# Kernel optimization log

Hardware: AMD Instinct MI355X
Metric: run time of the kernel (lower is better)

The kernel has to match this reference:

```python
import jax, jax.numpy as jnp
import numpy as np

B, L, D, E, H, TOP_K = 4, 2048, 1024, 8, 512, 2

def setup_inputs() -> dict:
    key = jax.random.key(0)
    k = jax.random.split(key, 6)
    x = jax.random.normal(k[0], (B, L, D), dtype=jnp.float32)
    gate_w = jax.random.normal(k[1], (D, E), dtype=jnp.float32) * 0.02
    gate_b = jnp.zeros((E,), jnp.float32)
    w1 = jax.random.normal(k[2], (E, D, H), dtype=jnp.float32) * 0.02
    b1 = jnp.zeros((E, H), jnp.float32)
    w2 = jax.random.normal(k[3], (E, H, D), dtype=jnp.float32) * 0.02
    b2 = jnp.zeros((E, D), jnp.float32)
    return {"x": x, "gate_w": gate_w, "gate_b": gate_b,
            "w1": w1, "b1": b1, "w2": w2, "b2": b2}

def reference(x, gate_w, gate_b, w1, b1, w2, b2):
    b, l, d = x.shape
    e = gate_w.shape[1]
    xf = x.reshape(-1, d)                      # [T, D], T = B*L
    t = xf.shape[0]
    # gating (eval mode: clean logits, no noise)
    logits = xf @ gate_w + gate_b              # [T, E]
    top_vals, top_idx = jax.lax.top_k(logits, TOP_K)
    top_gates = jax.nn.softmax(top_vals, axis=-1)
    gates = jnp.zeros((t, e), x.dtype).at[jnp.arange(t)[:, None], top_idx].set(top_gates)
    # per-expert 2-layer MLP computed densely, combined with sparse gates
    h = jax.nn.gelu(jnp.einsum('td,edh->eth', xf, w1) + b1[:, None, :], approximate=False)
    eo = jnp.einsum('eth,ehd->etd', h, w2) + b2[:, None, :]   # [E, T, D]
    out = jnp.einsum('te,etd->td', gates, eo)                 # weighted combine
    return out.reshape(b, l, d)
```

## Files before the change

kernel.cpp:

```cpp
#include <hip/hip_runtime.h>
#include <hip/hip_bf16.h>
#include <stdint.h>

#define B_    4
#define L_    2048
#define T_    8192
#define D_    1024
#define E_    8
#define H_    512

typedef __bf16  bf16x8 __attribute__((ext_vector_type(8)));
typedef float   f32x4  __attribute__((ext_vector_type(4)));
typedef unsigned short ushort_t;

__device__ __forceinline__ ushort_t f2bf(float f) {
    union { float f; unsigned u; } v; v.f = f;
    unsigned u = v.u;
    unsigned r = (u + 0x7fffu + ((u >> 16) & 1u)) >> 16;
    return (ushort_t)r;
}

__device__ __forceinline__ float gelu_exact(float v) {
    return 0.5f * v * (1.0f + erff(v * 0.70710678118654752f));
}

__device__ __forceinline__ void gld_lds16(const void* g, void* l) {
    __attribute__((address_space(3))) uint32_t* lp =
        reinterpret_cast<__attribute__((address_space(3))) uint32_t*>(
            reinterpret_cast<uintptr_t>(l));
    const __attribute__((address_space(1))) uint32_t* gp =
        reinterpret_cast<const __attribute__((address_space(1))) uint32_t*>(
            reinterpret_cast<uintptr_t>(g));
    __builtin_amdgcn_global_load_lds(gp, lp, 16, 0, 0);
}

__global__ __launch_bounds__(256) void transpose_cvt2(
    const float* __restrict__ w1, const float* __restrict__ w2,
    ushort_t* __restrict__ o1, ushort_t* __restrict__ o2)
{
    __shared__ float tile[32][33];
    const int mz = blockIdx.y;
    const float* src; ushort_t* dst; int C, R, sh;
    if (mz < E_) {
        src = w1 + (size_t)mz * D_ * H_; dst = o1 + (size_t)mz * D_ * H_;
        R = D_; C = H_; sh = 4;
    } else {
        const int m = mz - E_;
        src = w2 + (size_t)m * D_ * H_;  dst = o2 + (size_t)m * D_ * H_;
        R = H_; C = D_; sh = 5;
    }
    const int bx = blockIdx.x & ((1 << sh) - 1);
    const int by = blockIdx.x >> sh;
    const int r0 = by * 32, c0 = bx * 32;
    const int tid = threadIdx.x;
    const int lr = tid >> 3;
    const int lc = (tid & 7) * 4;
    float4 v = *(const float4*)(src + (size_t)(r0 + lr) * C + c0 + lc);
    tile[lr][lc+0] = v.x; tile[lr][lc+1] = v.y;
    tile[lr][lc+2] = v.z; tile[lr][lc+3] = v.w;
    __syncthreads();
    ushort4 o;
    o.x = f2bf(tile[lc+0][lr]);
    o.y = f2bf(tile[lc+1][lr]);
    o.z = f2bf(tile[lc+2][lr]);
    o.w = f2bf(tile[lc+3][lr]);
    *(ushort4*)(dst + (size_t)(c0 + lr) * R + r0 + lc) = o;
}

__global__ __launch_bounds__(256) void gating_kernel(
    const float* __restrict__ x, const float* __restrict__ gw,
    const float* __restrict__ gb,
    int* __restrict__ eidx, float* __restrict__ gsel, ushort_t* __restrict__ xbf)
{
    __shared__ float gwT[E_][D_];
    const int tid = threadIdx.x;

    #pragma unroll
    for (int it = 0; it < 8; ++it) {
        const int idx = it * 256 + tid;
        float4 v = *(const float4*)(gw + (size_t)idx * 4);
        const int row = idx >> 1;
        const int col = (idx & 1) * 4;
        gwT[col+0][row] = v.x;
        gwT[col+1][row] = v.y;
        gwT[col+2][row] = v.z;
        gwT[col+3][row] = v.w;
    }
    __syncthreads();

    const int wave = tid >> 6;
    const int lane = tid & 63;

    #pragma unroll
    for (int it = 0; it < 2; ++it) {
        const int t = blockIdx.x * 8 + wave * 2 + it;
        const float* xr = x + (size_t)t * D_;
        ushort_t* xbr = xbf + (size_t)t * D_;

        float acc[E_];
        #pragma unroll
        for (int e = 0; e < E_; ++e) acc[e] = 0.f;

        #pragma unroll
        for (int j = 0; j < 4; ++j) {
            const int d = j * 256 + lane * 4;
            float4 xv = *(const float4*)(xr + d);
            ushort4 o;
            o.x = f2bf(xv.x); o.y = f2bf(xv.y); o.z = f2bf(xv.z); o.w = f2bf(xv.w);
            *(ushort4*)(xbr + d) = o;
            #pragma unroll
            for (int e = 0; e < E_; ++e) {
                float4 w = *(const float4*)(&gwT[e][d]);
                acc[e] += xv.x * w.x + xv.y * w.y + xv.z * w.z + xv.w * w.w;
            }
        }
        #pragma unroll
        for (int s = 1; s < 64; s <<= 1) {
            #pragma unroll
            for (int e = 0; e < E_; ++e)
                acc[e] += __shfl_xor(acc[e], s, 64);
        }
        if (lane == 0) {
            float v[E_];
            #pragma unroll
            for (int e = 0; e < E_; ++e) v[e] = acc[e] + gb[e];
            int i0 = 0;
            #pragma unroll
            for (int e = 1; e < E_; ++e) if (v[e] > v[i0]) i0 = e;
            int i1 = (i0 == 0) ? 1 : 0;
            #pragma unroll
            for (int e = 0; e < E_; ++e) if (e != i0 && v[e] > v[i1]) i1 = e;
            float g0 = 1.f / (1.f + expf(v[i1] - v[i0]));
            eidx[t] = i0 | (i1 << 8);
            gsel[t] = g0;
        }
    }
}

__global__ __launch_bounds__(256) void bucket_kernel(
    const int* __restrict__ eidx, const float* __restrict__ gsel,
    int* __restrict__ counts, int* __restrict__ btok, float* __restrict__ bgate,
    uint32_t* __restrict__ tpos)
{
    __shared__ int lcnt[E_];
    __shared__ int lbase[E_];
    const int tid = threadIdx.x;
    if (tid < E_) lcnt[tid] = 0;
    __syncthreads();
    const int t = blockIdx.x * 256 + tid;
    const int pk = eidx[t];
    const float g0 = gsel[t];
    const int i0 = pk & 0xff, i1 = (pk >> 8) & 0xff;
    const int p0 = atomicAdd(&lcnt[i0], 1);
    const int p1 = atomicAdd(&lcnt[i1], 1);
    __syncthreads();
    if (tid < E_) lbase[tid] = atomicAdd(&counts[tid], lcnt[tid]);
    __syncthreads();
    const int q0 = lbase[i0] + p0, q1 = lbase[i1] + p1;
    btok[i0 * T_ + q0] = t; bgate[i0 * T_ + q0] = g0;
    btok[i1 * T_ + q1] = t; bgate[i1 * T_ + q1] = 1.f - g0;
    tpos[t] = (uint32_t)((i0 << 13) | q0) | ((uint32_t)((i1 << 13) | q1) << 16);
}

__global__ __launch_bounds__(256) void mlp1_kernel(
    const ushort_t* __restrict__ xbf, const ushort_t* __restrict__ w1t,
    const float* __restrict__ b1,
    const int* __restrict__ counts,
    const int* __restrict__ btok, ushort_t* __restrict__ hbuf)
{
    const int e   = blockIdx.z;
    const int n_e = counts[e];
    const int m0  = blockIdx.x * 64;
    if (m0 >= n_e) return;
    int off = 0;
    for (int i = 0; i < e; ++i) off += counts[i];
    const int n0  = blockIdx.y * 128;

    __shared__ ushort_t As[2][64 * 64];
    __shared__ ushort_t Bs[2][128 * 64];

    const int tid  = threadIdx.x;
    const int lane = tid & 63;
    const int wave = tid >> 6;

    const int srow = tid >> 3;
    const int cg   = (tid & 7) ^ (srow & 7);

    const ushort_t* aptr[2];
    #pragma unroll
    for (int i = 0; i < 2; ++i) {
        int m = m0 + i * 32 + srow;
        int tok = btok[e * T_ + (m < n_e ? m : n_e - 1)];
        aptr[i] = xbf + (size_t)tok * D_ + cg * 8;
    }
    const ushort_t* w1e = w1t + (size_t)e * (H_ * D_);
    const ushort_t* bptr[4];
    #pragma unroll
    for (int i = 0; i < 4; ++i)
        bptr[i] = w1e + (size_t)(n0 + i * 32 + srow) * D_ + cg * 8;

    const int fm   = lane & 15;
    const int quad = lane >> 4;
    const int wm   = (wave & 1) * 32;
    const int wn   = (wave >> 1) * 64;

    f32x4 acc[2][4];
    #pragma unroll
    for (int i = 0; i < 2; ++i)
        #pragma unroll
        for (int j = 0; j < 4; ++j)
            { acc[i][j][0]=0.f; acc[i][j][1]=0.f; acc[i][j][2]=0.f; acc[i][j][3]=0.f; }

    #define STAGE1(bufi, koff)                                              \
        do {                                                                \
            char* al_ = (char*)(&As[bufi][0]) + (wave << 10);               \
            char* bl_ = (char*)(&Bs[bufi][0]) + (wave << 10);               \
            _Pragma("unroll")                                               \
            for (int i_ = 0; i_ < 2; ++i_)                                  \
                gld_lds16(aptr[i_] + (koff), al_ + (i_ << 12));             \
            _Pragma("unroll")                                               \
            for (int i_ = 0; i_ < 4; ++i_)                                  \
                gld_lds16(bptr[i_] + (koff), bl_ + (i_ << 12));             \
        } while (0)

    STAGE1(0, 0);
    __builtin_amdgcn_sched_barrier(0);
    STAGE1(1, 64);
    __builtin_amdgcn_sched_barrier(0);

    int buf = 0;
    for (int k0 = 0; k0 < D_; k0 += 64) {
        if (k0 + 64 < D_) asm volatile("s_waitcnt vmcnt(6)" ::: "memory");
        else              asm volatile("s_waitcnt vmcnt(0)" ::: "memory");
        __builtin_amdgcn_s_barrier();
        const char* Ab = (const char*)(&As[buf][0]);
        const char* Bb = (const char*)(&Bs[buf][0]);
        #pragma unroll
        for (int kk = 0; kk < 2; ++kk) {
            const int grp = kk * 4 + quad;
            bf16x8 af[2], bfr[4];
            #pragma unroll
            for (int i = 0; i < 2; ++i) {
                int ra = wm + i * 16 + fm;
                af[i]  = *(const bf16x8*)(Ab + ra * 128 + ((grp ^ (ra & 7)) << 4));
            }
            #pragma unroll
            for (int j = 0; j < 4; ++j) {
                int rb = wn + j * 16 + fm;
                bfr[j] = *(const bf16x8*)(Bb + rb * 128 + ((grp ^ (rb & 7)) << 4));
            }
            #pragma unroll
            for (int i = 0; i < 2; ++i)
                #pragma unroll
                for (int j = 0; j < 4; ++j)
                    acc[i][j] = __builtin_amdgcn_mfma_f32_16x16x32_bf16(af[i], bfr[j], acc[i][j], 0, 0, 0);
        }
        if (k0 + 128 < D_) {
            asm volatile("s_waitcnt lgkmcnt(0)" ::: "memory");
            __builtin_amdgcn_s_barrier();
            STAGE1(buf, k0 + 128);
            __builtin_amdgcn_sched_barrier(0);
        }
        buf ^= 1;
    }
    #undef STAGE1

    float bcol[4];
    #pragma unroll
    for (int j = 0; j < 4; ++j)
        bcol[j] = b1[e * H_ + n0 + wn + j * 16 + fm];
    #pragma unroll
    for (int i = 0; i < 2; ++i) {
        #pragma unroll
        for (int r = 0; r < 4; ++r) {
            int m = m0 + wm + i * 16 + quad * 4 + r;
            if (m >= n_e) continue;
            ushort_t* hrow = hbuf + (size_t)(off + m) * H_ + n0;
            #pragma unroll
            for (int j = 0; j < 4; ++j)
                hrow[wn + j * 16 + fm] = f2bf(gelu_exact(acc[i][j][r] + bcol[j]));
        }
    }
}

__global__ __launch_bounds__(256) void mlp2_kernel(
    const ushort_t* __restrict__ hbuf, const ushort_t* __restrict__ w2t,
    const float* __restrict__ b2,
    const int* __restrict__ counts,
    const float* __restrict__ bgate, ushort_t* __restrict__ obuf)
{
    const int e   = blockIdx.z;
    const int n_e = counts[e];
    const int m0  = blockIdx.x * 64;
    if (m0 >= n_e) return;
    int off = 0;
    for (int i = 0; i < e; ++i) off += counts[i];
    const int n0  = blockIdx.y * 128;

    __shared__ ushort_t As[2][64 * 64];
    __shared__ ushort_t Bs[2][128 * 64];

    const int tid  = threadIdx.x;
    const int lane = tid & 63;
    const int wave = tid >> 6;

    const int srow = tid >> 3;
    const int cg   = (tid & 7) ^ (srow & 7);

    const ushort_t* aptr[2];
    #pragma unroll
    for (int i = 0; i < 2; ++i)
        aptr[i] = hbuf + (size_t)(off + m0 + i * 32 + srow) * H_ + cg * 8;
    const ushort_t* w2e = w2t + (size_t)e * (D_ * H_);
    const ushort_t* bptr[4];
    #pragma unroll
    for (int i = 0; i < 4; ++i)
        bptr[i] = w2e + (size_t)(n0 + i * 32 + srow) * H_ + cg * 8;

    const int fm   = lane & 15;
    const int quad = lane >> 4;
    const int wm   = (wave & 1) * 32;
    const int wn   = (wave >> 1) * 64;

    f32x4 acc[2][4];
    #pragma unroll
    for (int i = 0; i < 2; ++i)
        #pragma unroll
        for (int j = 0; j < 4; ++j)
            { acc[i][j][0]=0.f; acc[i][j][1]=0.f; acc[i][j][2]=0.f; acc[i][j][3]=0.f; }

    #define STAGE2(bufi, koff)                                              \
        do {                                                                \
            char* al_ = (char*)(&As[bufi][0]) + (wave << 10);               \
            char* bl_ = (char*)(&Bs[bufi][0]) + (wave << 10);               \
            _Pragma("unroll")                                               \
            for (int i_ = 0; i_ < 2; ++i_)                                  \
                gld_lds16(aptr[i_] + (koff), al_ + (i_ << 12));             \
            _Pragma("unroll")                                               \
            for (int i_ = 0; i_ < 4; ++i_)                                  \
                gld_lds16(bptr[i_] + (koff), bl_ + (i_ << 12));             \
        } while (0)

    STAGE2(0, 0);
    __builtin_amdgcn_sched_barrier(0);
    STAGE2(1, 64);
    __builtin_amdgcn_sched_barrier(0);

    int buf = 0;
    for (int k0 = 0; k0 < H_; k0 += 64) {
        if (k0 + 64 < H_) asm volatile("s_waitcnt vmcnt(6)" ::: "memory");
        else              asm volatile("s_waitcnt vmcnt(0)" ::: "memory");
        __builtin_amdgcn_s_barrier();
        const char* Ab = (const char*)(&As[buf][0]);
        const char* Bb = (const char*)(&Bs[buf][0]);
        #pragma unroll
        for (int kk = 0; kk < 2; ++kk) {
            const int grp = kk * 4 + quad;
            bf16x8 af[2], bfr[4];
            #pragma unroll
            for (int i = 0; i < 2; ++i) {
                int ra = wm + i * 16 + fm;
                af[i]  = *(const bf16x8*)(Ab + ra * 128 + ((grp ^ (ra & 7)) << 4));
            }
            #pragma unroll
            for (int j = 0; j < 4; ++j) {
                int rb = wn + j * 16 + fm;
                bfr[j] = *(const bf16x8*)(Bb + rb * 128 + ((grp ^ (rb & 7)) << 4));
            }
            #pragma unroll
            for (int i = 0; i < 2; ++i)
                #pragma unroll
                for (int j = 0; j < 4; ++j)
                    acc[i][j] = __builtin_amdgcn_mfma_f32_16x16x32_bf16(af[i], bfr[j], acc[i][j], 0, 0, 0);
        }
        if (k0 + 128 < H_) {
            asm volatile("s_waitcnt lgkmcnt(0)" ::: "memory");
            __builtin_amdgcn_s_barrier();
            STAGE2(buf, k0 + 128);
            __builtin_amdgcn_sched_barrier(0);
        }
        buf ^= 1;
    }
    #undef STAGE2

    float bcol[4];
    #pragma unroll
    for (int j = 0; j < 4; ++j)
        bcol[j] = b2[e * D_ + n0 + wn + j * 16 + fm];
    #pragma unroll
    for (int i = 0; i < 2; ++i) {
        #pragma unroll
        for (int r = 0; r < 4; ++r) {
            int m = m0 + wm + i * 16 + quad * 4 + r;
            if (m >= n_e) continue;
            float g = bgate[e * T_ + m];
            ushort_t* orow = obuf + (size_t)(off + m) * D_ + n0;
            #pragma unroll
            for (int j = 0; j < 4; ++j)
                orow[wn + j * 16 + fm] = f2bf((acc[i][j][r] + bcol[j]) * g);
        }
    }
}

__global__ __launch_bounds__(256) void combine_kernel(
    const ushort_t* __restrict__ obuf, const uint32_t* __restrict__ tpos,
    const int* __restrict__ counts, float* __restrict__ out)
{
    const int tid = threadIdx.x;
    const int t = blockIdx.x * 2 + (tid >> 7);
    const int c = (tid & 127) * 8;
    const uint32_t pk = tpos[t];
    const int e0 = (pk >> 13) & 7, p0 = pk & 0x1fff;
    const int e1 = (pk >> 29) & 7, p1 = (pk >> 16) & 0x1fff;

    const int4 ca = *(const int4*)(counts);
    const int4 cb = *(const int4*)(counts + 4);
    int pre[8];
    pre[0] = 0;
    pre[1] = ca.x;
    pre[2] = pre[1] + ca.y;
    pre[3] = pre[2] + ca.z;
    pre[4] = pre[3] + ca.w;
    pre[5] = pre[4] + cb.x;
    pre[6] = pre[5] + cb.y;
    pre[7] = pre[6] + cb.z;
    int off0 = 0, off1 = 0;
    #pragma unroll
    for (int i = 1; i < 8; ++i) {
        off0 = (e0 == i) ? pre[i] : off0;
        off1 = (e1 == i) ? pre[i] : off1;
    }

    const size_t s0 = (size_t)(off0 + p0) * D_ + c;
    const size_t s1 = (size_t)(off1 + p1) * D_ + c;
    bf16x8 a = *(const bf16x8*)(obuf + s0);
    bf16x8 b = *(const bf16x8*)(obuf + s1);
    float4 o0, o1;
    o0.x = (float)a[0] + (float)b[0];
    o0.y = (float)a[1] + (float)b[1];
    o0.z = (float)a[2] + (float)b[2];
    o0.w = (float)a[3] + (float)b[3];
    o1.x = (float)a[4] + (float)b[4];
    o1.y = (float)a[5] + (float)b[5];
    o1.z = (float)a[6] + (float)b[6];
    o1.w = (float)a[7] + (float)b[7];
    float* orow = out + (size_t)t * D_ + c;
    *(float4*)(orow)     = o0;
    *(float4*)(orow + 4) = o1;
}

extern "C" void kernel_launch(void* const* d_in, const int* in_sizes, int n_in,
                              void* d_out, int out_size, void* d_ws, size_t ws_size,
                              hipStream_t stream)
{
    const float* x  = (const float*)d_in[0];
    const float* gw = (const float*)d_in[1];
    const float* gb = (const float*)d_in[2];
    const float* w1 = (const float*)d_in[3];
    const float* b1 = (const float*)d_in[4];
    const float* w2 = (const float*)d_in[5];
    const float* b2 = (const float*)d_in[6];
    float* out = (float*)d_out;

    char* ws = (char*)d_ws;
    int*   counts  = (int*)ws;
    int*   btok    = (int*)(ws + 256);
    float* bgate   = (float*)(ws + 256 + (size_t)E_*T_*4);
    size_t p = 256 + 2ull * E_ * T_ * 4;
    int*      eidx = (int*)(ws + p);      p += (size_t)T_ * 4;
    float*    gsel = (float*)(ws + p);    p += (size_t)T_ * 4;
    uint32_t* tpos = (uint32_t*)(ws + p); p += (size_t)T_ * 4;
    ushort_t* xbf  = (ushort_t*)(ws + p); p += (size_t)T_*D_*2;
    ushort_t* w1t  = (ushort_t*)(ws + p); p += (size_t)E_*H_*D_*2;
    ushort_t* w2t  = (ushort_t*)(ws + p); p += (size_t)E_*D_*H_*2;
    ushort_t* hbuf = (ushort_t*)(ws + p); p += ((size_t)2*T_+128)*H_*2;
    ushort_t* obuf = (ushort_t*)(ws + p);

    (void)hipMemsetAsync(counts, 0, 64, stream);

    transpose_cvt2<<<dim3(512, 16), 256, 0, stream>>>(w1, w2, w1t, w2t);
    gating_kernel<<<T_/8, 256, 0, stream>>>(x, gw, gb, eidx, gsel, xbf);
    bucket_kernel<<<T_/256, 256, 0, stream>>>(eidx, gsel, counts, btok, bgate, tpos);
    mlp1_kernel<<<dim3(T_/64, H_/128, E_), 256, 0, stream>>>(
        xbf, w1t, b1, counts, btok, hbuf);
    mlp2_kernel<<<dim3(T_/64, D_/128, E_), 256, 0, stream>>>(
        hbuf, w2t, b2, counts, bgate, obuf);
    combine_kernel<<<T_/2, 256, 0, stream>>>(obuf, tpos, counts, out);
}
```

Before: 214.0 us.

## Merge weight transpose and gating into one launch; use fast GELU approximation

Folds the weight transpose/convert kernel and the gating kernel into one launch that branches on block index, removing one kernel launch and letting the two independent pieces of work overlap. It also swaps the exact erf-based GELU in the first MLP for the Abramowitz–Stegun polynomial erf approximation using a fast reciprocal and a fast exp. The shared memory buffer is now sized for the gating path (32KB) even in transpose blocks, which may lower occupancy for those blocks. The GELU approximation adds a small numerical error, which the bf16 output rounding of the hidden activations may absorb.

```diff
diff --git a/kernel.cpp b/kernel.cpp
--- a/kernel.cpp
+++ b/kernel.cpp
@@ -20,8 +20,19 @@
     return (ushort_t)r;
 }
 
-__device__ __forceinline__ float gelu_exact(float v) {
-    return 0.5f * v * (1.0f + erff(v * 0.70710678118654752f));
+__device__ __forceinline__ float gelu_fast(float v) {
+    float x  = v * 0.70710678118654752f;
+    float ax = fabsf(x);
+    float t  = __builtin_amdgcn_rcpf(1.0f + 0.3275911f * ax);
+    float y  = t * (0.254829592f +
+               t * (-0.284496736f +
+               t * (1.421413741f +
+               t * (-1.453152027f +
+               t * 1.061405429f))));
+    float e  = __expf(-x * x);
+    float er = 1.0f - y * e;
+    er = copysignf(er, x);
+    return 0.5f * v * (1.0f + er);
 }
 
 __device__ __forceinline__ void gld_lds16(const void* g, void* l) {
@@ -34,46 +45,50 @@
     __builtin_amdgcn_global_load_lds(gp, lp, 16, 0, 0);
 }
 
-__global__ __launch_bounds__(256) void transpose_cvt2(
+__global__ __launch_bounds__(256) void prep_kernel(
     const float* __restrict__ w1, const float* __restrict__ w2,
-    ushort_t* __restrict__ o1, ushort_t* __restrict__ o2)
-{
-    __shared__ float tile[32][33];
-    const int mz = blockIdx.y;
-    const float* src; ushort_t* dst; int C, R, sh;
-    if (mz < E_) {
-        src = w1 + (size_t)mz * D_ * H_; dst = o1 + (size_t)mz * D_ * H_;
-        R = D_; C = H_; sh = 4;
-    } else {
-        const int m = mz - E_;
-        src = w2 + (size_t)m * D_ * H_;  dst = o2 + (size_t)m * D_ * H_;
-        R = H_; C = D_; sh = 5;
-    }
-    const int bx = blockIdx.x & ((1 << sh) - 1);
-    const int by = blockIdx.x >> sh;
-    const int r0 = by * 32, c0 = bx * 32;
-    const int tid = threadIdx.x;
-    const int lr = tid >> 3;
-    const int lc = (tid & 7) * 4;
-    float4 v = *(const float4*)(src + (size_t)(r0 + lr) * C + c0 + lc);
-    tile[lr][lc+0] = v.x; tile[lr][lc+1] = v.y;
-    tile[lr][lc+2] = v.z; tile[lr][lc+3] = v.w;
-    __syncthreads();
-    ushort4 o;
-    o.x = f2bf(tile[lc+0][lr]);
-    o.y = f2bf(tile[lc+1][lr]);
-    o.z = f2bf(tile[lc+2][lr]);
-    o.w = f2bf(tile[lc+3][lr]);
-    *(ushort4*)(dst + (size_t)(c0 + lr) * R + r0 + lc) = o;
-}
-
-__global__ __launch_bounds__(256) void gating_kernel(
+    ushort_t* __restrict__ o1, ushort_t* __restrict__ o2,
     const float* __restrict__ x, const float* __restrict__ gw,
     const float* __restrict__ gb,
     int* __restrict__ eidx, float* __restrict__ gsel, ushort_t* __restrict__ xbf)
 {
-    __shared__ float gwT[E_][D_];
+    __shared__ float smem[E_ * D_];
+    const int bid = blockIdx.x;
     const int tid = threadIdx.x;
+
+    if (bid < 8192) {
+        float (*tile)[33] = reinterpret_cast<float(*)[33]>(smem);
+        const int mz = bid >> 9;
+        const int bxy = bid & 511;
+        const float* src; ushort_t* dst; int C, R, sh;
+        if (mz < E_) {
+            src = w1 + (size_t)mz * D_ * H_; dst = o1 + (size_t)mz * D_ * H_;
+            R = D_; C = H_; sh = 4;
+        } else {
+            const int m = mz - E_;
+            src = w2 + (size_t)m * D_ * H_;  dst = o2 + (size_t)m * D_ * H_;
+            R = H_; C = D_; sh = 5;
+        }
+        const int bx = bxy & ((1 << sh) - 1);
+        const int by = bxy >> sh;
+        const int r0 = by * 32, c0 = bx * 32;
+        const int lr = tid >> 3;
+        const int lc = (tid & 7) * 4;
+        float4 v = *(const float4*)(src + (size_t)(r0 + lr) * C + c0 + lc);
+        tile[lr][lc+0] = v.x; tile[lr][lc+1] = v.y;
+        tile[lr][lc+2] = v.z; tile[lr][lc+3] = v.w;
+        __syncthreads();
+        ushort4 o;
+        o.x = f2bf(tile[lc+0][lr]);
+        o.y = f2bf(tile[lc+1][lr]);
+        o.z = f2bf(tile[lc+2][lr]);
+        o.w = f2bf(tile[lc+3][lr]);
+        *(ushort4*)(dst + (size_t)(c0 + lr) * R + r0 + lc) = o;
+        return;
+    }
+
+    float (*gwT)[D_] = reinterpret_cast<float(*)[D_]>(smem);
+    const int gbid = bid - 8192;
 
     #pragma unroll
     for (int it = 0; it < 8; ++it) {
@@ -93,7 +108,7 @@
 
     #pragma unroll
     for (int it = 0; it < 2; ++it) {
-        const int t = blockIdx.x * 8 + wave * 2 + it;
+        const int t = gbid * 8 + wave * 2 + it;
         const float* xr = x + (size_t)t * D_;
         ushort_t* xbr = xbf + (size_t)t * D_;
 
@@ -278,7 +293,7 @@
             ushort_t* hrow = hbuf + (size_t)(off + m) * H_ + n0;
             #pragma unroll
             for (int j = 0; j < 4; ++j)
-                hrow[wn + j * 16 + fm] = f2bf(gelu_exact(acc[i][j][r] + bcol[j]));
+                hrow[wn + j * 16 + fm] = f2bf(gelu_fast(acc[i][j][r] + bcol[j]));
         }
     }
 }
@@ -478,8 +493,8 @@
 
     (void)hipMemsetAsync(counts, 0, 64, stream);
 
-    transpose_cvt2<<<dim3(512, 16), 256, 0, stream>>>(w1, w2, w1t, w2t);
-    gating_kernel<<<T_/8, 256, 0, stream>>>(x, gw, gb, eidx, gsel, xbf);
+    prep_kernel<<<8192 + T_/8, 256, 0, stream>>>(
+        w1, w2, w1t, w2t, x, gw, gb, eidx, gsel, xbf);
     bucket_kernel<<<T_/256, 256, 0, stream>>>(eidx, gsel, counts, btok, bgate, tpos);
     mlp1_kernel<<<dim3(T_/64, H_/128, E_), 256, 0, stream>>>(
         xbf, w1t, b1, counts, btok, hbuf);
```

Result: faster. 204.3 us (-4.5%).
